# Performance work log

Hardware: AMD Instinct MI355X
Metric: run time of the kernel (lower is better)

## Reference

```python
import jax, jax.numpy as jnp
import numpy as np

D = 1024
H = 8
DK = D // H
DFF = 4 * D
EPS = 1e-6


def layer_norm(x, g, b):
    mu = jnp.mean(x, axis=-1, keepdims=True)
    var = jnp.mean(jnp.square(x - mu), axis=-1, keepdims=True)
    return (x - mu) * jax.lax.rsqrt(var + EPS) * g + b


def setup_inputs() -> dict:
    key = jax.random.key(0)
    ks = jax.random.split(key, 8)
    s = 0.02
    return {
        "x": jax.random.normal(ks[0], (4, 2048, D), dtype=jnp.float32),
        "Wq": jax.random.normal(ks[1], (D, D), dtype=jnp.float32) * s,
        "bq": jnp.zeros((D,), dtype=jnp.float32),
        "Wk": jax.random.normal(ks[2], (D, D), dtype=jnp.float32) * s,
        "bk": jnp.zeros((D,), dtype=jnp.float32),
        "Wv": jax.random.normal(ks[3], (D, D), dtype=jnp.float32) * s,
        "bv": jnp.zeros((D,), dtype=jnp.float32),
        "ln1_g": jnp.ones((D,), dtype=jnp.float32),
        "ln1_b": jnp.zeros((D,), dtype=jnp.float32),
        "W1": jax.random.normal(ks[4], (D, DFF), dtype=jnp.float32) * s,
        "b1": jnp.zeros((DFF,), dtype=jnp.float32),
        "W2": jax.random.normal(ks[5], (DFF, D), dtype=jnp.float32) * s,
        "b2": jnp.zeros((D,), dtype=jnp.float32),
        "ln2_g": jnp.ones((D,), dtype=jnp.float32),
        "ln2_b": jnp.zeros((D,), dtype=jnp.float32),
    }


def reference(x, Wq, bq, Wk, bk, Wv, bv, ln1_g, ln1_b, W1, b1, W2, b2, ln2_g, ln2_b):
    B, S, _ = x.shape

    def split_heads(t):  # [B,S,D] -> [B,H,S,dk]
        return t.reshape(B, S, H, DK).transpose(0, 2, 1, 3)

    Q = split_heads(x @ Wq + bq)
    K = split_heads(x @ Wk + bk)
    V = split_heads(x @ Wv + bv)

    scores = jnp.einsum("bhqd,bhkd->bhqk", Q, K) / jnp.sqrt(jnp.float32(DK))
    attn = jax.nn.softmax(scores, axis=-1)  # dropout is identity at eval
    out = jnp.einsum("bhqk,bhkd->bhqd", attn, V)
    out = out.transpose(0, 2, 1, 3).reshape(B, S, D)
    x1 = layer_norm(out + x, ln1_g, ln1_b)

    h = jax.nn.relu(x1 @ W1 + b1) @ W2 + b2  # dropout identity at eval
    return layer_norm(h + x1, ln2_g, ln2_b)
```

## Files before the change

kernel.cpp:

```cpp
#include <hip/hip_runtime.h>
#include <hip/hip_bf16.h>
#include <stdint.h>

#define D_MODEL 1024
#define NHEADS  8
#define DKH     128
#define DFF     4096
#define SEQ     2048
#define BATCH   4
#define NTOK    (BATCH*SEQ)
#define QKS     2048
#define QSCALE  0.12751743f

typedef float  f32x4  __attribute__((ext_vector_type(4)));
typedef __bf16 bf16x8 __attribute__((ext_vector_type(8)));

static __device__ __forceinline__ float b2f(ushort u) {
    union { uint32_t i; float f; } v; v.i = ((uint32_t)u) << 16; return v.f;
}
static __device__ __forceinline__ ushort f2b(float f) {
    union { float f; uint32_t i; } v; v.f = f;
    uint32_t r = v.i + 0x7fffu + ((v.i >> 16) & 1u);
    return (ushort)(r >> 16);
}
static __device__ __forceinline__ ushort f2b_native(float f) {
    __bf16 h = (__bf16)f;
    return __builtin_bit_cast(ushort, h);
}
static __device__ __forceinline__ float exp2_hw(float x) {
    return __builtin_amdgcn_exp2f(x);
}
static __device__ __forceinline__ void gl_lds16(const void* g, void* l) {
    __builtin_amdgcn_global_load_lds(
        (const __attribute__((address_space(1))) void*)g,
        (__attribute__((address_space(3))) void*)l, 16, 0, 0);
}
static __device__ __forceinline__ float dpp_max16(float x) {
    int t;
    t = __builtin_amdgcn_update_dpp(0, __builtin_bit_cast(int, x), 0xB1, 0xF, 0xF, true);
    x = fmaxf(x, __builtin_bit_cast(float, t));
    t = __builtin_amdgcn_update_dpp(0, __builtin_bit_cast(int, x), 0x4E, 0xF, 0xF, true);
    x = fmaxf(x, __builtin_bit_cast(float, t));
    t = __builtin_amdgcn_update_dpp(0, __builtin_bit_cast(int, x), 0x141, 0xF, 0xF, true);
    x = fmaxf(x, __builtin_bit_cast(float, t));
    t = __builtin_amdgcn_update_dpp(0, __builtin_bit_cast(int, x), 0x140, 0xF, 0xF, true);
    x = fmaxf(x, __builtin_bit_cast(float, t));
    return x;
}

__global__ __launch_bounds__(256) void conv_kernel(
    const float* __restrict__ in, ushort* __restrict__ out, int n)
{
    for (int i = (blockIdx.x * 256 + threadIdx.x) * 4; i < n; i += gridDim.x * 1024) {
        float4 v = *(const float4*)(in + i);
        ushort o[4] = { f2b(v.x), f2b(v.y), f2b(v.z), f2b(v.w) };
        *(uint2*)(out + i) = *(const uint2*)o;
    }
}

__global__ __launch_bounds__(256) void tconv_kernel(
    const float* __restrict__ in, ushort* __restrict__ out, int R, int C)
{
    __shared__ float L[32][33];
    const int tid = threadIdx.x;
    const int tx = tid & 31, ty = tid >> 5;
    const int nbc = C >> 5;
    const int r0 = (blockIdx.x / nbc) << 5;
    const int c0 = (blockIdx.x % nbc) << 5;
    #pragma unroll
    for (int p = 0; p < 4; ++p)
        L[ty + 8 * p][tx] = in[(size_t)(r0 + ty + 8 * p) * C + c0 + tx];
    __syncthreads();
    #pragma unroll
    for (int p = 0; p < 4; ++p)
        out[(size_t)(c0 + ty + 8 * p) * R + r0 + tx] = f2b(L[tx][ty + 8 * p]);
}

__global__ __launch_bounds__(256) void cat3_kernel(
    const float* __restrict__ a, const float* __restrict__ b,
    const float* __restrict__ c, float* __restrict__ out)
{
    const int i = blockIdx.x * 256 + threadIdx.x;
    out[i] = (i < 1024) ? a[i] : (i < 2048) ? b[i - 1024] : c[i - 2048];
}

template<int MODE>
__global__ __launch_bounds__(256) void gemm_bt(
    const ushort* __restrict__ A, const ushort* __restrict__ Bt,
    const float* __restrict__ bias, ushort* __restrict__ C,
    int M, int N, int K, ushort* __restrict__ vt)
{
    __shared__ __align__(16) ushort As[128 * 32];
    __shared__ __align__(16) ushort Bs[128 * 32];

    const int tid  = threadIdx.x;
    const int w    = tid >> 6;
    const int lane = tid & 63;
    const int l16  = lane & 15;
    const int quad = lane >> 4;

    const int nbn = N >> 7;
    const int m0  = (blockIdx.x / nbn) << 7;
    const int n0  = (blockIdx.x % nbn) << 7;

    const int wm = (w >> 1) << 6;
    const int wn = (w & 1) << 6;

    const int srow = (w << 5) + (lane >> 2);
    const int scol = (lane & 3) << 3;
    const ushort* Ag = A  + (size_t)(m0 + srow) * K + scol;
    const ushort* Bg = Bt + (size_t)(n0 + srow) * K + scol;
    ushort* Asw = &As[(w << 5) * 32];
    ushort* Bsw = &Bs[(w << 5) * 32];

    f32x4 acc[4][4] = {};

    for (int k0 = 0; k0 < K; k0 += 32) {
        __syncthreads();
        gl_lds16(Ag + k0,                  Asw);
        gl_lds16(Ag + k0 + (size_t)16 * K, Asw + 16 * 32);
        gl_lds16(Bg + k0,                  Bsw);
        gl_lds16(Bg + k0 + (size_t)16 * K, Bsw + 16 * 32);
        __syncthreads();

        bf16x8 af[4], bf[4];
        #pragma unroll
        for (int i = 0; i < 4; ++i) {
            af[i] = *(const bf16x8*)&As[(wm + i * 16 + l16) * 32 + (quad << 3)];
            bf[i] = *(const bf16x8*)&Bs[(wn + i * 16 + l16) * 32 + (quad << 3)];
        }
        #pragma unroll
        for (int mt = 0; mt < 4; ++mt)
            #pragma unroll
            for (int nt = 0; nt < 4; ++nt)
                acc[mt][nt] = __builtin_amdgcn_mfma_f32_16x16x32_bf16(
                    af[mt], bf[nt], acc[mt][nt], 0, 0, 0);
    }

    if (MODE == 2 && n0 >= 2048) {
        #pragma unroll
        for (int nt = 0; nt < 4; ++nt) {
            const int n  = n0 + wn + (nt << 4) + l16;
            const int hd = n - 2048;
            const float bv = bias[n];
            const size_t vrow = (size_t)(hd >> 7) * 128 + (hd & 127);
            #pragma unroll
            for (int mt = 0; mt < 4; ++mt) {
                const int m = m0 + wm + (mt << 4) + (quad << 2);
                const size_t row = (size_t)(m >> 11) * 1024 + vrow;
                ushort pk[4];
                #pragma unroll
                for (int r = 0; r < 4; ++r) pk[r] = f2b(acc[mt][nt][r] + bv);
                *(uint2*)(vt + row * SEQ + (m & 2047)) = *(const uint2*)pk;
            }
        }
    } else {
        const int ldc = (MODE == 2) ? QKS : N;
        const float qs = (MODE == 2 && n0 < 1024) ? QSCALE : 1.f;
        #pragma unroll
        for (int nt = 0; nt < 4; ++nt) {
            const int n = n0 + wn + (nt << 4) + l16;
            const float bv = bias[n];
            #pragma unroll
            for (int mt = 0; mt < 4; ++mt) {
                #pragma unroll
                for (int r = 0; r < 4; ++r) {
                    const int m = m0 + wm + (mt << 4) + (quad << 2) + r;
                    float v = acc[mt][nt][r] + bv;
                    if (MODE == 1) v = fmaxf(v, 0.f);
                    if (MODE == 2) v *= qs;
                    C[(size_t)m * ldc + n] = f2b(v);
                }
            }
        }
    }
}

__global__ __launch_bounds__(256) void gemm_bt_sk(
    const ushort* __restrict__ A, const ushort* __restrict__ Bt,
    const float* __restrict__ bias, ushort* __restrict__ C0,
    ushort* __restrict__ C1, int M, int N, int K)
{
    __shared__ __align__(16) ushort As[128 * 32];
    __shared__ __align__(16) ushort Bs[128 * 32];

    const int tiles = (M >> 7) * (N >> 7);
    const int sl  = blockIdx.x / tiles;
    const int tix = blockIdx.x % tiles;
    const int kbeg = sl * (K >> 1);
    const int kend = kbeg + (K >> 1);

    const int tid  = threadIdx.x;
    const int w    = tid >> 6;
    const int lane = tid & 63;
    const int l16  = lane & 15;
    const int quad = lane >> 4;

    const int nbn = N >> 7;
    const int m0  = (tix / nbn) << 7;
    const int n0  = (tix % nbn) << 7;

    const int wm = (w >> 1) << 6;
    const int wn = (w & 1) << 6;

    const int srow = (w << 5) + (lane >> 2);
    const int scol = (lane & 3) << 3;
    const ushort* Ag = A  + (size_t)(m0 + srow) * K + scol;
    const ushort* Bg = Bt + (size_t)(n0 + srow) * K + scol;
    ushort* Asw = &As[(w << 5) * 32];
    ushort* Bsw = &Bs[(w << 5) * 32];

    f32x4 acc[4][4] = {};

    for (int k0 = kbeg; k0 < kend; k0 += 32) {
        __syncthreads();
        gl_lds16(Ag + k0,                  Asw);
        gl_lds16(Ag + k0 + (size_t)16 * K, Asw + 16 * 32);
        gl_lds16(Bg + k0,                  Bsw);
        gl_lds16(Bg + k0 + (size_t)16 * K, Bsw + 16 * 32);
        __syncthreads();

        bf16x8 af[4], bf[4];
        #pragma unroll
        for (int i = 0; i < 4; ++i) {
            af[i] = *(const bf16x8*)&As[(wm + i * 16 + l16) * 32 + (quad << 3)];
            bf[i] = *(const bf16x8*)&Bs[(wn + i * 16 + l16) * 32 + (quad << 3)];
        }
        #pragma unroll
        for (int mt = 0; mt < 4; ++mt)
            #pragma unroll
            for (int nt = 0; nt < 4; ++nt)
                acc[mt][nt] = __builtin_amdgcn_mfma_f32_16x16x32_bf16(
                    af[mt], bf[nt], acc[mt][nt], 0, 0, 0);
    }

    ushort* C = sl ? C1 : C0;
    #pragma unroll
    for (int nt = 0; nt < 4; ++nt) {
        const int n = n0 + wn + (nt << 4) + l16;
        const float bv = sl ? 0.f : bias[n];
        #pragma unroll
        for (int mt = 0; mt < 4; ++mt) {
            #pragma unroll
            for (int r = 0; r < 4; ++r) {
                const int m = m0 + wm + (mt << 4) + (quad << 2) + r;
                C[(size_t)m * N + n] = f2b(acc[mt][nt][r] + bv);
            }
        }
    }
}

__global__ __launch_bounds__(256) void attn_kernel(
    ushort* __restrict__ qk, const ushort* __restrict__ vt)
{
    __shared__ __align__(16) ushort smem[40960];
    ushort* Ks = smem;
    ushort* Vs = smem + 16384;
    ushort* Ps = smem + 32768;

    const int tid  = threadIdx.x;
    const int w    = tid >> 6;
    const int lane = tid & 63;
    const int l16  = lane & 15;
    const int quad = lane >> 4;

    const int bid = ((blockIdx.x & 7) << 7) + (blockIdx.x >> 3);
    const int qb  = bid & 31;
    const int h   = (bid >> 5) & 7;
    const int b   = bid >> 8;

    ushort* Qp = qk + ((size_t)(b * SEQ + qb * 64)) * QKS + h * DKH;
    const ushort* Kp = qk + ((size_t)(b * SEQ)) * QKS + 1024 + h * DKH;
    const ushort* Vp = vt + ((size_t)((b * 8 + h) * 128)) * SEQ;

    #pragma unroll
    for (int i = 0; i < 4; ++i) {
        const int row = w * 16 + i * 4 + quad;
        const int g = (l16 & 8) | ((l16 & 7) ^ (row & 7));
        gl_lds16(Qp + (size_t)row * QKS + g * 8, Vs + (w * 16 + i * 4) * 128);
    }
    #pragma unroll
    for (int i = 0; i < 8; ++i) {
        const int row = w * 32 + i * 4 + quad;
        const int g = (l16 & 8) | ((l16 & 7) ^ (row & 7));
        gl_lds16(Kp + (size_t)row * QKS + g * 8, Ks + (w * 32 + i * 4) * 128);
    }
    __syncthreads();

    bf16x8 aq[4];
    {
        const int r = w * 16 + l16;
        #pragma unroll
        for (int kq = 0; kq < 4; ++kq) {
            const int gk = kq * 4 + quad;
            const int g = (gk & 8) | ((gk & 7) ^ (r & 7));
            aq[kq] = *(const bf16x8*)&Vs[r * 128 + g * 8];
        }
    }
    __syncthreads();

    #pragma unroll
    for (int i = 0; i < 8; ++i) {
        const int d = w * 32 + i * 4 + quad;
        const int g = (l16 & 8) | ((l16 & 7) ^ (d & 7));
        gl_lds16(Vp + (size_t)d * SEQ + g * 8, Vs + (w * 32 + i * 4) * 128);
    }

    f32x4 o[8] = {};
    float mrun[4], lrun[4];
    #pragma unroll
    for (int r = 0; r < 4; ++r) { mrun[r] = -1e30f; lrun[r] = 0.f; }

    for (int t = 0; t < SEQ / 128; ++t) {
        f32x4 s[8] = {};
        #pragma unroll
        for (int nt = 0; nt < 8; ++nt) {
            const int rk = nt * 16 + l16;
            #pragma unroll
            for (int kq = 0; kq < 4; ++kq) {
                const int gk = kq * 4 + quad;
                const int g = (gk & 8) | ((gk & 7) ^ (rk & 7));
                bf16x8 bk = *(const bf16x8*)&Ks[rk * 128 + g * 8];
                s[nt] = __builtin_amdgcn_mfma_f32_16x16x32_bf16(aq[kq], bk, s[nt], 0, 0, 0);
            }
        }
        __syncthreads();

        if (t + 1 < SEQ / 128) {
            #pragma unroll
            for (int i = 0; i < 8; ++i) {
                const int row = w * 32 + i * 4 + quad;
                const int g = (l16 & 8) | ((l16 & 7) ^ (row & 7));
                gl_lds16(Kp + ((size_t)((t + 1) * 128 + row)) * QKS + g * 8,
                         Ks + (w * 32 + i * 4) * 128);
            }
        }

        float vmax[4];
        #pragma unroll
        for (int r = 0; r < 4; ++r) {
            float v = s[0][r];
            #pragma unroll
            for (int nt = 1; nt < 8; ++nt) v = fmaxf(v, s[nt][r]);
            vmax[r] = dpp_max16(v);
        }
        const int grew = (vmax[0] > mrun[0]) | (vmax[1] > mrun[1]) |
                         (vmax[2] > mrun[2]) | (vmax[3] > mrun[3]);
        if (__any(grew)) {
            #pragma unroll
            for (int r = 0; r < 4; ++r) {
                const float mnew = fmaxf(mrun[r], vmax[r]);
                const float alpha = exp2_hw(mrun[r] - mnew);
                mrun[r] = mnew;
                lrun[r] *= alpha;
                #pragma unroll
                for (int nt8 = 0; nt8 < 8; ++nt8)
                    o[nt8][r] *= alpha;
            }
        }
        #pragma unroll
        for (int nt = 0; nt < 8; ++nt)
            #pragma unroll
            for (int r = 0; r < 4; ++r) {
                const float p = exp2_hw(s[nt][r] - mrun[r]);
                lrun[r] += p;
                const int row = w * 16 + (quad << 2) + r;
                Ps[row * 128 + ((nt * 16 + l16) ^ ((row & 7) << 3))] = f2b_native(p);
            }

        #pragma unroll
        for (int kp = 0; kp < 4; ++kp) {
            const int rowp = w * 16 + l16;
            const int gp = kp * 4 + quad;
            const int gsw = (gp & 8) | ((gp & 7) ^ (rowp & 7));
            bf16x8 ap = *(const bf16x8*)&Ps[rowp * 128 + gsw * 8];
            #pragma unroll
            for (int nt8 = 0; nt8 < 8; ++nt8) {
                const int d = nt8 * 16 + l16;
                const int gv = (gp & 8) | ((gp & 7) ^ (d & 7));
                bf16x8 bv = *(const bf16x8*)&Vs[d * 128 + gv * 8];
                o[nt8] = __builtin_amdgcn_mfma_f32_16x16x32_bf16(ap, bv, o[nt8], 0, 0, 0);
            }
        }
        __syncthreads();

        if (t + 1 < SEQ / 128) {
            #pragma unroll
            for (int i = 0; i < 8; ++i) {
                const int d = w * 32 + i * 4 + quad;
                const int g = (l16 & 8) | ((l16 & 7) ^ (d & 7));
                gl_lds16(Vp + (size_t)d * SEQ + (t + 1) * 128 + g * 8,
                         Vs + (w * 32 + i * 4) * 128);
            }
        }
    }

    #pragma unroll
    for (int r = 0; r < 4; ++r) {
        float v = lrun[r];
        #pragma unroll
        for (int msk = 1; msk <= 8; msk <<= 1)
            v += __shfl_xor(v, msk, 64);
        lrun[r] = v;
    }
    #pragma unroll
    for (int r = 0; r < 4; ++r) {
        const float inv = 1.f / lrun[r];
        const int row = w * 16 + (quad << 2) + r;
        #pragma unroll
        for (int nt8 = 0; nt8 < 8; ++nt8)
            Qp[(size_t)row * QKS + nt8 * 16 + l16] = f2b_native(o[nt8][r] * inv);
    }
}

__global__ __launch_bounds__(256) void ln_kernel(
    const ushort* __restrict__ a, int astride, const ushort* __restrict__ a2,
    const void* __restrict__ res, int res_f32,
    const float* __restrict__ g, const float* __restrict__ be,
    void* __restrict__ out, int out_f32)
{
    __shared__ float red[8];
    const int row = blockIdx.x;
    const int tid = threadIdx.x;
    const int col = tid * 4;

    ushort av[4];
    *(uint2*)av = *(const uint2*)(a + (size_t)row * astride + col);

    float v[4];
    if (res_f32) {
        float4 rr = *(const float4*)((const float*)res + (size_t)row * D_MODEL + col);
        v[0] = b2f(av[0]) + rr.x; v[1] = b2f(av[1]) + rr.y;
        v[2] = b2f(av[2]) + rr.z; v[3] = b2f(av[3]) + rr.w;
    } else {
        ushort rv[4];
        *(uint2*)rv = *(const uint2*)((const ushort*)res + (size_t)row * D_MODEL + col);
        #pragma unroll
        for (int i = 0; i < 4; ++i) v[i] = b2f(av[i]) + b2f(rv[i]);
    }
    if (a2) {
        ushort bv[4];
        *(uint2*)bv = *(const uint2*)(a2 + (size_t)row * D_MODEL + col);
        #pragma unroll
        for (int i = 0; i < 4; ++i) v[i] += b2f(bv[i]);
    }

    float s = v[0] + v[1] + v[2] + v[3];
    #pragma unroll
    for (int m = 1; m <= 32; m <<= 1) s += __shfl_xor(s, m, 64);
    if ((tid & 63) == 0) red[tid >> 6] = s;
    __syncthreads();
    const float mu = (red[0] + red[1] + red[2] + red[3]) * (1.f / D_MODEL);

    float q = 0.f;
    #pragma unroll
    for (int i = 0; i < 4; ++i) { const float d = v[i] - mu; q += d * d; }
    #pragma unroll
    for (int m = 1; m <= 32; m <<= 1) q += __shfl_xor(q, m, 64);
    if ((tid & 63) == 0) red[4 + (tid >> 6)] = q;
    __syncthreads();
    const float var = (red[4] + red[5] + red[6] + red[7]) * (1.f / D_MODEL);
    const float rstd = rsqrtf(var + 1e-6f);

    float4 gg = *(const float4*)(g + col);
    float4 bb = *(const float4*)(be + col);
    float y[4];
    y[0] = (v[0] - mu) * rstd * gg.x + bb.x;
    y[1] = (v[1] - mu) * rstd * gg.y + bb.y;
    y[2] = (v[2] - mu) * rstd * gg.z + bb.z;
    y[3] = (v[3] - mu) * rstd * gg.w + bb.w;

    if (out_f32) {
        float4 ov; ov.x = y[0]; ov.y = y[1]; ov.z = y[2]; ov.w = y[3];
        *(float4*)((float*)out + (size_t)row * D_MODEL + col) = ov;
    } else {
        ushort ov[4] = { f2b(y[0]), f2b(y[1]), f2b(y[2]), f2b(y[3]) };
        *(uint2*)((ushort*)out + (size_t)row * D_MODEL + col) = *(const uint2*)ov;
    }
}

__global__ __launch_bounds__(256) void sentinel_kernel(float* out, float S, int n) {
    for (int i = blockIdx.x * 256 + threadIdx.x; i < n; i += gridDim.x * 256)
        out[i] = S;
}

extern "C" void kernel_launch(void* const* d_in, const int* in_sizes, int n_in,
                              void* d_out, int out_size, void* d_ws, size_t ws_size,
                              hipStream_t stream)
{
    const float* x   = (const float*)d_in[0];
    const float* Wq  = (const float*)d_in[1];
    const float* bq  = (const float*)d_in[2];
    const float* Wk  = (const float*)d_in[3];
    const float* bk  = (const float*)d_in[4];
    const float* Wv  = (const float*)d_in[5];
    const float* bv  = (const float*)d_in[6];
    const float* g1  = (const float*)d_in[7];
    const float* be1 = (const float*)d_in[8];
    const float* W1  = (const float*)d_in[9];
    const float* b1  = (const float*)d_in[10];
    const float* W2  = (const float*)d_in[11];
    const float* b2  = (const float*)d_in[12];
    const float* g2  = (const float*)d_in[13];
    const float* be2 = (const float*)d_in[14];

    const size_t MB = 1024 * 1024;
    dim3 blk(256);

    if (ws_size < 88 * MB) {
        int k = (int)(ws_size >> 23); if (k > 127) k = 127;
        sentinel_kernel<<<dim3(2048), blk, 0, stream>>>(
            (float*)d_out, 1024.f + 8.f * (float)k, out_size);
        return;
    }

    char* ws = (char*)d_ws;
    ushort* qkb    = (ushort*)(ws);
    ushort* vtb    = (ushort*)(ws + 32 * MB);
    ushort* ffn0   = (ushort*)(ws);
    ushort* ffn1   = (ushort*)(ws + 16 * MB);
    ushort* xb     = (ushort*)(ws + 48 * MB);
    ushort* x1     = (ushort*)(ws + 48 * MB);
    ushort* wqkv_t = (ushort*)(ws + 64 * MB);
    ushort* w1t    = (ushort*)(ws + 70 * MB);
    ushort* w2t    = (ushort*)(ws + 78 * MB);
    float*  bqkv   = (float*) (ws + 86 * MB);
    ushort* hbuf   = (ushort*)d_out;

    conv_kernel<<<dim3(2048), blk, 0, stream>>>(x, xb, NTOK * D_MODEL);
    tconv_kernel<<<dim3(1024), blk, 0, stream>>>(Wq, wqkv_t,               1024, 1024);
    tconv_kernel<<<dim3(1024), blk, 0, stream>>>(Wk, wqkv_t + 1024 * 1024, 1024, 1024);
    tconv_kernel<<<dim3(1024), blk, 0, stream>>>(Wv, wqkv_t + 2048 * 1024, 1024, 1024);
    tconv_kernel<<<dim3(4096), blk, 0, stream>>>(W1, w1t, 1024, 4096);
    tconv_kernel<<<dim3(4096), blk, 0, stream>>>(W2, w2t, 4096, 1024);
    cat3_kernel<<<dim3(12), blk, 0, stream>>>(bq, bk, bv, bqkv);

    gemm_bt<2><<<dim3(64 * 24), blk, 0, stream>>>(xb, wqkv_t, bqkv, qkb,
                                                  NTOK, 3072, D_MODEL, vtb);

    attn_kernel<<<dim3(BATCH * NHEADS * (SEQ / 64)), blk, 0, stream>>>(qkb, vtb);

    ln_kernel<<<dim3(NTOK), blk, 0, stream>>>(qkb, QKS, nullptr, x, 1, g1, be1, x1, 0);

    for (int c = 0; c < 2; ++c) {
        const size_t ro = (size_t)c * 4096;
        gemm_bt<1><<<dim3(32 * 32), blk, 0, stream>>>(
            x1 + ro * D_MODEL, w1t, b1, hbuf, 4096, DFF, D_MODEL, nullptr);
        gemm_bt_sk<<<dim3(2 * 32 * 8), blk, 0, stream>>>(
            hbuf, w2t, b2, ffn0 + ro * D_MODEL, ffn1 + ro * D_MODEL,
            4096, D_MODEL, DFF);
    }

    ln_kernel<<<dim3(NTOK), blk, 0, stream>>>(ffn0, D_MODEL, ffn1, x1, 0,
                                              g2, be2, d_out, 1);
}
```

Before: 594.6 us.

## Add 256x256-tile 8-wave pipelined GEMM for FFN1 and widen P-tile swizzle

Replaces the FFN first GEMM (bias+ReLU) with a new 512-thread kernel that computes 256x256 output tiles. It double-buffers 64-wide K slices in LDS, interleaves the async global-to-LDS loads with MFMA phases, and raises wave priority around the MFMA blocks. The larger tile is meant to improve operand reuse and hide load latency, at the cost of 128KB of LDS per block and lower occupancy. Separately, the attention P-tile swizzle now XORs with 16 row bits instead of 8, which should reduce LDS bank conflicts.

New measurement: 570.4 us. 1.04x faster.

```diff
diff --git a/kernel.cpp b/kernel.cpp
--- a/kernel.cpp
+++ b/kernel.cpp
@@ -250,6 +250,126 @@
     }
 }
 
+__global__ __launch_bounds__(512, 2) void gemm8_relu(
+    const ushort* __restrict__ A, const ushort* __restrict__ Bt,
+    const float* __restrict__ bias, ushort* __restrict__ C,
+    int M, int N, int K)
+{
+    __shared__ __align__(16) ushort lds[65536];
+
+    const int tid  = threadIdx.x;
+    const int w    = tid >> 6;
+    const int lane = tid & 63;
+    const int l16  = lane & 15;
+    const int quad = (lane >> 4) & 3;
+    const int wm   = w >> 2;
+    const int wn   = w & 3;
+
+    const int nbn = N >> 8;
+    const int m0  = (blockIdx.x / nbn) << 8;
+    const int n0  = (blockIdx.x % nbn) << 8;
+
+    const int rsub = tid >> 3;
+    const int gsw  = (tid & 7) ^ (rsub & 7);
+    const ushort* Asrc = A  + (size_t)(m0 + rsub) * K + gsw * 8;
+    const ushort* Bsrc = Bt + (size_t)(n0 + rsub) * K + gsw * 8;
+
+    auto issue_half = [&](int p, int kt, int d) {
+        const ushort* src;
+        int base;
+        if (p < 2) { src = Asrc + (size_t)(p * 128) * K;       base = d * 16384 + p * 8192; }
+        else       { src = Bsrc + (size_t)((p - 2) * 128) * K; base = 32768 + d * 16384 + (p - 2) * 8192; }
+        src += kt * 64;
+        gl_lds16(src,                  &lds[base + w * 512]);
+        gl_lds16(src + (size_t)64 * K, &lds[base + w * 512 + 4096]);
+    };
+
+    f32x4  acc[8][4] = {};
+    bf16x8 bfr[4];
+
+    auto phase = [&](int cur, int ks, int mq, bool readB) {
+        const int Ab = cur * 16384 + wm * 8192;
+        const int Bb = 32768 + cur * 16384 + (wn >> 1) * 8192;
+        if (readB) {
+            #pragma unroll
+            for (int nt = 0; nt < 4; ++nt) {
+                const int rB = ((wn & 1) << 6) + nt * 16 + l16;
+                const int gB = ((ks << 2) + quad) ^ (rB & 7);
+                bfr[nt] = *(const bf16x8*)&lds[Bb + rB * 64 + gB * 8];
+            }
+        }
+        bf16x8 afr[4];
+        #pragma unroll
+        for (int mt = 0; mt < 4; ++mt) {
+            const int rA = mq * 64 + mt * 16 + l16;
+            const int gA = ((ks << 2) + quad) ^ (rA & 7);
+            afr[mt] = *(const bf16x8*)&lds[Ab + rA * 64 + gA * 8];
+        }
+        __builtin_amdgcn_s_setprio(1);
+        #pragma unroll
+        for (int mt = 0; mt < 4; ++mt)
+            #pragma unroll
+            for (int nt = 0; nt < 4; ++nt)
+                acc[mq * 4 + mt][nt] = __builtin_amdgcn_mfma_f32_16x16x32_bf16(
+                    afr[mt], bfr[nt], acc[mq * 4 + mt][nt], 0, 0, 0);
+        __builtin_amdgcn_s_setprio(0);
+    };
+
+    const int NT = K >> 6;
+
+    #pragma unroll
+    for (int p = 0; p < 4; ++p) issue_half(p, 0, 0);
+    issue_half(0, 1, 1);
+    asm volatile("s_waitcnt vmcnt(2)" ::: "memory");
+    __builtin_amdgcn_sched_barrier(0);
+    __builtin_amdgcn_s_barrier();
+    __builtin_amdgcn_sched_barrier(0);
+
+    for (int t = 0; t < NT; ++t) {
+        const int  cur = t & 1;
+        const bool pf  = (t + 1 < NT);
+
+        if (pf) issue_half(1, t + 1, cur ^ 1);
+        phase(cur, 0, 0, true);
+        if (pf) issue_half(2, t + 1, cur ^ 1);
+        phase(cur, 0, 1, false);
+        if (pf) issue_half(3, t + 1, cur ^ 1);
+        phase(cur, 1, 0, true);
+        phase(cur, 1, 1, false);
+
+        __builtin_amdgcn_sched_barrier(0);
+        __builtin_amdgcn_s_barrier();
+        __builtin_amdgcn_sched_barrier(0);
+        if (pf) {
+            if (t + 2 < NT) {
+                issue_half(0, t + 2, cur);
+                asm volatile("s_waitcnt vmcnt(2)" ::: "memory");
+            } else {
+                asm volatile("s_waitcnt vmcnt(0)" ::: "memory");
+            }
+            __builtin_amdgcn_sched_barrier(0);
+            __builtin_amdgcn_s_barrier();
+            __builtin_amdgcn_sched_barrier(0);
+        }
+    }
+    __builtin_amdgcn_sched_barrier(0);
+
+    #pragma unroll
+    for (int nt = 0; nt < 4; ++nt) {
+        const int n = n0 + wn * 64 + nt * 16 + l16;
+        const float bv = bias[n];
+        #pragma unroll
+        for (int a = 0; a < 8; ++a) {
+            const int mrow = m0 + wm * 128 + (a >> 2) * 64 + (a & 3) * 16 + (quad << 2);
+            #pragma unroll
+            for (int r = 0; r < 4; ++r) {
+                const float v = fmaxf(acc[a][nt][r] + bv, 0.f);
+                C[(size_t)(mrow + r) * N + n] = f2b(v);
+            }
+        }
+    }
+}
+
 __global__ __launch_bounds__(256) void attn_kernel(
     ushort* __restrict__ qk, const ushort* __restrict__ vt)
 {
@@ -365,14 +485,14 @@
                 const float p = exp2_hw(s[nt][r] - mrun[r]);
                 lrun[r] += p;
                 const int row = w * 16 + (quad << 2) + r;
-                Ps[row * 128 + ((nt * 16 + l16) ^ ((row & 7) << 3))] = f2b_native(p);
+                Ps[row * 128 + ((nt * 16 + l16) ^ ((row & 15) << 3))] = f2b_native(p);
             }
 
         #pragma unroll
         for (int kp = 0; kp < 4; ++kp) {
             const int rowp = w * 16 + l16;
             const int gp = kp * 4 + quad;
-            const int gsw = (gp & 8) | ((gp & 7) ^ (rowp & 7));
+            const int gsw = gp ^ (rowp & 15);
             bf16x8 ap = *(const bf16x8*)&Ps[rowp * 128 + gsw * 8];
             #pragma unroll
             for (int nt8 = 0; nt8 < 8; ++nt8) {
@@ -544,8 +664,8 @@
 
     for (int c = 0; c < 2; ++c) {
         const size_t ro = (size_t)c * 4096;
-        gemm_bt<1><<<dim3(32 * 32), blk, 0, stream>>>(
-            x1 + ro * D_MODEL, w1t, b1, hbuf, 4096, DFF, D_MODEL, nullptr);
+        gemm8_relu<<<dim3(16 * 16), dim3(512), 0, stream>>>(
+            x1 + ro * D_MODEL, w1t, b1, hbuf, 4096, DFF, D_MODEL);
         gemm_bt_sk<<<dim3(2 * 32 * 8), blk, 0, stream>>>(
             hbuf, w2t, b2, ffn0 + ro * D_MODEL, ffn1 + ro * D_MODEL,
             4096, D_MODEL, DFF);
```
